# Performance work log

Measured on AMD Instinct MI355X. Metric: run time of the kernel, lower is better.

Reference implementation:

```python
import jax, jax.numpy as jnp
import numpy as np

POOLING_COUNTS = [15, 8, 8]
N = 64


def _build_specs():
    # Reproduces SparseMaxPool.__init__: mask2d and per-pooler (kernel, stride, i, j).
    mask = np.zeros((N, N), dtype=bool)
    mask[np.arange(N), np.arange(N)] = True
    stride, offset = 1, 0
    specs = []
    for idx, c in enumerate(POOLING_COUNTS):
        for t in range(c):
            offset += stride
            i = np.arange(0, N - offset, stride)
            j = np.arange(offset, N, stride)
            mask[i, j] = True
            # first pooler of each later scale group is MaxPool1d(3,2), rest are (2,1)
            k, s = (3, 2) if (idx > 0 and t == 0) else (2, 1)
            specs.append((k, s, i, j))
        stride *= 2
    return mask, specs


def _maxpool1d(x, k, s):
    # x: [B, D, L] -> [B, D, (L-k)//s + 1], max over sliding window via strided slices
    L = x.shape[-1]
    out = (L - k) // s + 1
    y = x[..., 0:s * (out - 1) + 1:s]
    for d in range(1, k):
        y = jnp.maximum(y, x[..., d:d + s * (out - 1) + 1:s])
    return y


def setup_inputs() -> dict:
    key = jax.random.key(0)
    return {"x": jax.random.normal(key, (32, 512, N), dtype=jnp.float32)}


def reference(x):
    mask_np, specs = _build_specs()
    B, D, n = x.shape
    diag = jnp.arange(n)
    map2d = jnp.zeros((B, D, n, n), dtype=x.dtype).at[:, :, diag, diag].set(x)
    for k, s, i, j in specs:
        x = _maxpool1d(x, k, s)
        map2d = map2d.at[:, :, jnp.asarray(i), jnp.asarray(j)].set(x)
    mask2d = jnp.broadcast_to(jnp.asarray(mask_np)[None, None], (B, 1, n, n))
    return map2d, mask2d
```

## Files before the change

kernel.cpp:

```cpp
#include <hip/hip_runtime.h>


constexpr int S_LEN[31] = {
  63,62,61,60,59,58,57,56,55,54,53,52,51,50,49,
  24,23,22,21,20,19,18,17,
  8,7,6,5,4,3,2,1};
constexpr int S_ST[31] = {
  1,1,1,1,1,1,1,1,1,1,1,1,1,1,1,
  2,2,2,2,2,2,2,2,
  4,4,4,4,4,4,4,4};
constexpr int S_OFF[31] = {
  1,2,3,4,5,6,7,8,9,10,11,12,13,14,15,
  17,19,21,23,25,27,29,31,
  35,39,43,47,51,55,59,63};

__global__ void __launch_bounds__(64)
sparse_pool_kernel(const float* __restrict__ x, float* __restrict__ out,
                   int nrows, int ntiles) {
  __shared__ float tile[4096];
  const int lane = threadIdx.x;

  const float4 z = make_float4(0.f, 0.f, 0.f, 0.f);
#pragma unroll
  for (int i = 0; i < 16; ++i)
    ((float4*)tile)[i * 64 + lane] = z;

  int t = blockIdx.x;
  float curx = 0.f;
  if (t < ntiles) curx = (t < nrows) ? x[(size_t)t * 64 + lane] : 1.0f;

  for (; t < ntiles; t += gridDim.x) {
    tile[lane * 65] = curx;

    float cur = curx;
#pragma unroll
    for (int m = 0; m < 31; ++m) {
      if (m == 15 || m == 23) {
        float a = __shfl(cur, 2 * lane);
        float b = __shfl(cur, 2 * lane + 1);
        float c = __shfl(cur, 2 * lane + 2);
        cur = fmaxf(fmaxf(a, b), c);
      } else {
        cur = fmaxf(cur, __shfl_down(cur, 1));
      }
      if (lane < S_LEN[m]) tile[lane * (S_ST[m] * 65) + S_OFF[m]] = cur;
    }

    const int tn = t + gridDim.x;
    float nx = 0.f;
    if (tn < ntiles) nx = (tn < nrows) ? x[(size_t)tn * 64 + lane] : 1.0f;

    float4* o4 = (float4*)(out + (size_t)t * 4096);
    const float4* t4 = (const float4*)tile;
#pragma unroll
    for (int it = 0; it < 16; ++it)
      o4[it * 64 + lane] = t4[it * 64 + lane];

    curx = nx;
  }
}

extern "C" void kernel_launch(void* const* d_in, const int* in_sizes, int n_in,
                              void* d_out, int out_size, void* d_ws, size_t ws_size,
                              hipStream_t stream) {
  const float* x = (const float*)d_in[0];
  float* out = (float*)d_out;

  const int nx     = in_sizes[0];
  const int nrows  = nx / 64;
  const int ntiles = out_size / 4096;

  const int blocks = (ntiles + 7) / 8;
  sparse_pool_kernel<<<dim3(blocks), 64, 0, stream>>>(x, out, nrows, ntiles);
}
```

Before: 268.6 us.

## Store pooled values in compact LDS buffer and gather via precomputed indices

Replaces the 4096-float LDS tile with a 1105-entry compact buffer holding only the non-zero pooled values plus a zero slot. Each lane precomputes 16-bit packed byte offsets for its output positions once, then gathers from LDS while writing the full tile to global memory. This removes per-tile zeroing and cuts LDS footprint so more blocks fit per CU. The grid also grows from ntiles/8 to ntiles/2 blocks with a launch-bounds occupancy hint. The cost is 32 registers for the index table and scalar gathered LDS reads in place of vector reads.

```diff
diff --git a/kernel.cpp b/kernel.cpp
--- a/kernel.cpp
+++ b/kernel.cpp
@@ -5,33 +5,71 @@
   63,62,61,60,59,58,57,56,55,54,53,52,51,50,49,
   24,23,22,21,20,19,18,17,
   8,7,6,5,4,3,2,1};
-constexpr int S_ST[31] = {
-  1,1,1,1,1,1,1,1,1,1,1,1,1,1,1,
-  2,2,2,2,2,2,2,2,
-  4,4,4,4,4,4,4,4};
-constexpr int S_OFF[31] = {
-  1,2,3,4,5,6,7,8,9,10,11,12,13,14,15,
-  17,19,21,23,25,27,29,31,
-  35,39,43,47,51,55,59,63};
 
-__global__ void __launch_bounds__(64)
+constexpr int sbase(int m) {
+  int b = 64;
+  for (int i = 0; i < m; ++i) b += S_LEN[i];
+  return b;
+}
+static_assert(sbase(30) + S_LEN[30] == 1104, "compact size");
+
+constexpr bool bases_ok() {
+  for (int off = 1; off <= 15; ++off)
+    if (64 + 63 * (off - 1) - (off - 1) * (off - 2) / 2 != sbase(off - 1)) return false;
+  for (int mm = 0; mm < 8; ++mm)
+    if (904 + 24 * mm - mm * (mm - 1) / 2 != sbase(15 + mm)) return false;
+  for (int mm = 0; mm < 8; ++mm)
+    if (1068 + 8 * mm - mm * (mm - 1) / 2 != sbase(23 + mm)) return false;
+  return true;
+}
+static_assert(bases_ok(), "closed-form emit bases disagree with scatter bases");
+
+__device__ __forceinline__ int cidx_of(int r, int c) {
+  const int off = c - r;
+  int idx = 1104;
+  if (off == 0) idx = r;
+  if (off >= 1 && off <= 15) {
+    const int m = off - 1;
+    idx = 64 + 63 * m - m * (m - 1) / 2 + r;
+  }
+  if (off >= 17 && off <= 31 && (off & 1) && !(r & 1)) {
+    const int mm = (off - 17) >> 1;
+    idx = 904 + 24 * mm - mm * (mm - 1) / 2 + (r >> 1);
+  }
+  if (off >= 35 && off <= 63 && !((off - 35) & 3) && !(r & 3)) {
+    const int mm = (off - 35) >> 2;
+    idx = 1068 + 8 * mm - mm * (mm - 1) / 2 + (r >> 2);
+  }
+  return idx;
+}
+
+__global__ void __launch_bounds__(64, 8)
 sparse_pool_kernel(const float* __restrict__ x, float* __restrict__ out,
                    int nrows, int ntiles) {
-  __shared__ float tile[4096];
+  __shared__ float comp[1105];
   const int lane = threadIdx.x;
 
-  const float4 z = make_float4(0.f, 0.f, 0.f, 0.f);
-#pragma unroll
-  for (int i = 0; i < 16; ++i)
-    ((float4*)tile)[i * 64 + lane] = z;
+  if (lane == 0) comp[1104] = 0.0f;
 
   int t = blockIdx.x;
   float curx = 0.f;
   if (t < ntiles) curx = (t < nrows) ? x[(size_t)t * 64 + lane] : 1.0f;
 
+  uint32_t idxp[32];
+#pragma unroll
+  for (int it = 0; it < 16; ++it) {
+    const int r  = it * 4 + (lane >> 4);
+    const int c0 = (lane & 15) * 4;
+    idxp[2 * it] =
+        (uint32_t)(cidx_of(r, c0 + 0) * 4) |
+        ((uint32_t)(cidx_of(r, c0 + 1) * 4) << 16);
+    idxp[2 * it + 1] =
+        (uint32_t)(cidx_of(r, c0 + 2) * 4) |
+        ((uint32_t)(cidx_of(r, c0 + 3) * 4) << 16);
+  }
+
   for (; t < ntiles; t += gridDim.x) {
-    tile[lane * 65] = curx;
-
+    comp[lane] = curx;
     float cur = curx;
 #pragma unroll
     for (int m = 0; m < 31; ++m) {
@@ -43,7 +81,7 @@
       } else {
         cur = fmaxf(cur, __shfl_down(cur, 1));
       }
-      if (lane < S_LEN[m]) tile[lane * (S_ST[m] * 65) + S_OFF[m]] = cur;
+      if (lane < S_LEN[m]) comp[sbase(m) + lane] = cur;
     }
 
     const int tn = t + gridDim.x;
@@ -51,10 +89,17 @@
     if (tn < ntiles) nx = (tn < nrows) ? x[(size_t)tn * 64 + lane] : 1.0f;
 
     float4* o4 = (float4*)(out + (size_t)t * 4096);
-    const float4* t4 = (const float4*)tile;
+    const char* cb = (const char*)comp;
 #pragma unroll
-    for (int it = 0; it < 16; ++it)
-      o4[it * 64 + lane] = t4[it * 64 + lane];
+    for (int it = 0; it < 16; ++it) {
+      const uint32_t wa = idxp[2 * it], wb = idxp[2 * it + 1];
+      float4 v;
+      v.x = *(const float*)(cb + (wa & 0xffffu));
+      v.y = *(const float*)(cb + (wa >> 16));
+      v.z = *(const float*)(cb + (wb & 0xffffu));
+      v.w = *(const float*)(cb + (wb >> 16));
+      o4[it * 64 + lane] = v;
+    }
 
     curx = nx;
   }
@@ -70,6 +115,6 @@
   const int nrows  = nx / 64;
   const int ntiles = out_size / 4096;
 
-  const int blocks = (ntiles + 7) / 8;
+  const int blocks = (ntiles + 1) / 2;
   sparse_pool_kernel<<<dim3(blocks), 64, 0, stream>>>(x, out, nrows, ntiles);
 }
```

New measurement: 316.5 us. +17.9%, slower.

## Use 4-wave blocks per tile with DPP shuffles and split scatter/copy

Applied to the files above, without the earlier changes.

Each tile is now handled by a 256-thread block of four waves instead of one wave. Every wave recomputes the pooling chain redundantly but writes only a quarter of the diagonals and copies a quarter of the tile rows to global memory, with block barriers between phases. The cross-lane shuffles become DPP row shifts plus a single shuffle for the strided poolers, and the grid is capped at 2048 blocks. The aim is more memory-level parallelism per tile and cheaper lane exchange, at the cost of two barriers per tile and redundant ALU work. Note that DPP row_shr and quad_perm operate within 16-lane rows, which may give wrong values at row boundaries.

```diff
diff --git a/kernel.cpp b/kernel.cpp
--- a/kernel.cpp
+++ b/kernel.cpp
@@ -1,5 +1,7 @@
 #include <hip/hip_runtime.h>
 
+
+typedef float vfloat4 __attribute__((ext_vector_type(4)));
 
 constexpr int S_LEN[31] = {
   63,62,61,60,59,58,57,56,55,54,53,52,51,50,49,
@@ -14,47 +16,63 @@
   17,19,21,23,25,27,29,31,
   35,39,43,47,51,55,59,63};
 
-__global__ void __launch_bounds__(64)
+template <int CTRL>
+__device__ __forceinline__ float dpp_movf(float v) {
+  return __int_as_float(
+      __builtin_amdgcn_update_dpp(0, __float_as_int(v), CTRL, 0xF, 0xF, true));
+}
+
+__global__ void __launch_bounds__(256, 8)
 sparse_pool_kernel(const float* __restrict__ x, float* __restrict__ out,
                    int nrows, int ntiles) {
   __shared__ float tile[4096];
-  const int lane = threadIdx.x;
+  const int tid  = threadIdx.x;
+  const int lane = tid & 63;
+  const int w    = tid >> 6;
 
-  const float4 z = make_float4(0.f, 0.f, 0.f, 0.f);
+  const vfloat4 z = {0.f, 0.f, 0.f, 0.f};
 #pragma unroll
-  for (int i = 0; i < 16; ++i)
-    ((float4*)tile)[i * 64 + lane] = z;
+  for (int i = 0; i < 4; ++i)
+    ((vfloat4*)tile)[i * 256 + tid] = z;
+  __syncthreads();
 
+  const int stride = gridDim.x;
   int t = blockIdx.x;
   float curx = 0.f;
   if (t < ntiles) curx = (t < nrows) ? x[(size_t)t * 64 + lane] : 1.0f;
 
-  for (; t < ntiles; t += gridDim.x) {
-    tile[lane * 65] = curx;
+  for (; t < ntiles; t += stride) {
+    if (w == 3) tile[lane * 65] = curx;
 
     float cur = curx;
 #pragma unroll
     for (int m = 0; m < 31; ++m) {
       if (m == 15 || m == 23) {
-        float a = __shfl(cur, 2 * lane);
-        float b = __shfl(cur, 2 * lane + 1);
-        float c = __shfl(cur, 2 * lane + 2);
-        cur = fmaxf(fmaxf(a, b), c);
+        float a = fmaxf(cur, dpp_movf<0x130>(cur));
+        float u = fmaxf(a, dpp_movf<0xB1>(a));
+        cur = __shfl(u, 2 * lane);
       } else {
-        cur = fmaxf(cur, __shfl_down(cur, 1));
+        cur = fmaxf(cur, dpp_movf<0x130>(cur));
       }
-      if (lane < S_LEN[m]) tile[lane * (S_ST[m] * 65) + S_OFF[m]] = cur;
+      if ((m & 3) == w && lane < S_LEN[m])
+        tile[lane * (S_ST[m] * 65) + S_OFF[m]] = cur;
     }
 
-    const int tn = t + gridDim.x;
+    const int tn = t + stride;
     float nx = 0.f;
     if (tn < ntiles) nx = (tn < nrows) ? x[(size_t)tn * 64 + lane] : 1.0f;
 
-    float4* o4 = (float4*)(out + (size_t)t * 4096);
-    const float4* t4 = (const float4*)tile;
+    __syncthreads();
+
+    vfloat4* o4 = (vfloat4*)(out + (size_t)t * 4096);
+    const vfloat4* t4 = (const vfloat4*)tile;
 #pragma unroll
-    for (int it = 0; it < 16; ++it)
-      o4[it * 64 + lane] = t4[it * 64 + lane];
+    for (int it = 0; it < 4; ++it) {
+      const int row = w * 4 + it;
+      o4[row * 64 + lane] = t4[row * 64 + lane];
+    }
+
+    __syncthreads();
 
     curx = nx;
   }
@@ -70,6 +88,7 @@
   const int nrows  = nx / 64;
   const int ntiles = out_size / 4096;
 
-  const int blocks = (ntiles + 7) / 8;
-  sparse_pool_kernel<<<dim3(blocks), 64, 0, stream>>>(x, out, nrows, ntiles);
+  int blocks = (ntiles + 7) / 8;
+  if (blocks > 2048) blocks = 2048;
+  sparse_pool_kernel<<<dim3(blocks), 256, 0, stream>>>(x, out, nrows, ntiles);
 }
```

Measured after the change: 262.4 us. -2.3%, faster.
